# Performance work log

Measured on AMD Instinct MI355X. Metric: run time of the kernel, lower is better.

## Reference

```python
import jax, jax.numpy as jnp
import numpy as np

N_BUS = 200000; N_GEN = 50000
E_BB = 1600000; E_GB = 400000; E_BG = 400000
D_IN = 64; H = 32
OUT_BUS = 4; OUT_GEN = 2


def setup_inputs() -> dict:
    key = jax.random.key(0)
    it = iter(jax.random.split(key, 48))
    def nrm(shape, s=0.05):
        return jax.random.normal(next(it), shape, jnp.float32) * s
    inp = {}
    inp["x_bus"] = jax.random.normal(next(it), (N_BUS, D_IN), jnp.float32)
    inp["x_gen"] = jax.random.normal(next(it), (N_GEN, D_IN), jnp.float32)
    inp["src_bb"] = jax.random.randint(next(it), (E_BB,), 0, N_BUS)
    inp["dst_bb"] = jax.random.randint(next(it), (E_BB,), 0, N_BUS)
    inp["src_gb"] = jax.random.randint(next(it), (E_GB,), 0, N_GEN)
    inp["dst_gb"] = jax.random.randint(next(it), (E_GB,), 0, N_BUS)
    inp["src_bg"] = jax.random.randint(next(it), (E_BG,), 0, N_BUS)
    inp["dst_bg"] = jax.random.randint(next(it), (E_BG,), 0, N_GEN)
    # SAGEConv params per layer / relation: lin_l (on aggregated neighbors, with bias),
    # lin_r (root weight on x_dst, no bias) -- matches PyG SAGEConv defaults.
    for lname, din in (("l1", D_IN), ("l2", H)):
        for rel in ("bb", "gb", "bg"):
            inp[f"{lname}_{rel}_Wl"] = nrm((din, H))
            inp[f"{lname}_{rel}_bl"] = jnp.zeros((H,), jnp.float32)
            inp[f"{lname}_{rel}_Wr"] = nrm((din, H))
    for nt, dout in (("bus", OUT_BUS), ("gen", OUT_GEN)):
        inp[f"lin0_{nt}_W"] = nrm((H, H))
        inp[f"lin0_{nt}_b"] = jnp.zeros((H,), jnp.float32)
        inp[f"linf_{nt}_W"] = nrm((H, dout))
        inp[f"linf_{nt}_b"] = jnp.zeros((dout,), jnp.float32)
    return inp


def _sage(x_src, x_dst, src, dst, Wl, bl, Wr, n_dst):
    # SAGEConv: mean-aggregate neighbor features, then out = lin_l(mean) + lin_r(x_dst)
    msg = jax.ops.segment_sum(x_src[src], dst, num_segments=n_dst)
    cnt = jax.ops.segment_sum(jnp.ones((src.shape[0],), x_src.dtype), dst, num_segments=n_dst)
    mean = msg / jnp.maximum(cnt, 1.0)[:, None]
    return mean @ Wl + bl + x_dst @ Wr


def reference(x_bus, x_gen, src_bb, dst_bb, src_gb, dst_gb, src_bg, dst_bg,
              l1_bb_Wl, l1_bb_bl, l1_bb_Wr, l1_gb_Wl, l1_gb_bl, l1_gb_Wr,
              l1_bg_Wl, l1_bg_bl, l1_bg_Wr,
              l2_bb_Wl, l2_bb_bl, l2_bb_Wr, l2_gb_Wl, l2_gb_bl, l2_gb_Wr,
              l2_bg_Wl, l2_bg_bl, l2_bg_Wr,
              lin0_bus_W, lin0_bus_b, lin0_gen_W, lin0_gen_b,
              linf_bus_W, linf_bus_b, linf_gen_W, linf_gen_b):
    # HeteroConv layer 1 (aggr='sum' over relations targeting each dst type)
    hb = (_sage(x_bus, x_bus, src_bb, dst_bb, l1_bb_Wl, l1_bb_bl, l1_bb_Wr, N_BUS)
          + _sage(x_gen, x_bus, src_gb, dst_gb, l1_gb_Wl, l1_gb_bl, l1_gb_Wr, N_BUS))
    hg = _sage(x_bus, x_gen, src_bg, dst_bg, l1_bg_Wl, l1_bg_bl, l1_bg_Wr, N_GEN)
    xb, xg = jax.nn.relu(hb), jax.nn.relu(hg)  # dropout is identity in eval mode
    # HeteroConv layer 2
    hb = (_sage(xb, xb, src_bb, dst_bb, l2_bb_Wl, l2_bb_bl, l2_bb_Wr, N_BUS)
          + _sage(xg, xb, src_gb, dst_gb, l2_gb_Wl, l2_gb_bl, l2_gb_Wr, N_BUS))
    hg = _sage(xb, xg, src_bg, dst_bg, l2_bg_Wl, l2_bg_bl, l2_bg_Wr, N_GEN)
    xb, xg = jax.nn.relu(hb), jax.nn.relu(hg)
    # per-node-type hidden Linear (input relu'd again as in the original; relu is idempotent)
    xb = jax.nn.relu(xb) @ lin0_bus_W + lin0_bus_b
    xg = jax.nn.relu(xg) @ lin0_gen_W + lin0_gen_b
    out_bus = xb @ linf_bus_W + linf_bus_b
    out_gen = xg @ linf_gen_W + linf_gen_b
    return out_bus, out_gen
```

## Files before the change

kernel.cpp:

```cpp
#include <hip/hip_runtime.h>
#include <hip/hip_bf16.h>

#define N_BUS 200000
#define N_GEN 50000
#define E_BB 1600000
#define E_GB 400000
#define E_BG 400000
#define H 32
#define NBINS 1024
#define EPT 16

#define NBK_BUS 782
#define NBK_GEN 196
#define CAP_BB 2560
#define CAP_GB 768
#define CAP_BG 2560

#define NB_PART_BB 391
#define NB_PART_GB 98
#define NB_PART_BG 98
#define NB_PART_ALL 587
#define NB_TF_BUS 782
#define NB_TF_GEN 196
#define NB_PL_BUS 6250
#define NB_PL_GEN 1563

typedef __attribute__((ext_vector_type(8))) short short8;
typedef __attribute__((ext_vector_type(4))) float floatx4;

__device__ inline unsigned short f2bf(float f) {
    __hip_bfloat16 h = __float2bfloat16(f);
    return *reinterpret_cast<unsigned short*>(&h);
}
__device__ inline float bf2f(unsigned short u) {
    return __uint_as_float(((unsigned)u) << 16);
}

__device__ __forceinline__ void part_body(int blk, const int* __restrict__ src,
                                          const int* __restrict__ dst, int nE,
                                          unsigned* __restrict__ cnt, int CAP,
                                          unsigned* __restrict__ pairs) {
    __shared__ unsigned hist[NBINS];
    __shared__ unsigned base[NBINS];
    const int tid = threadIdx.x;
    const int cbase = blk * (256 * EPT);

    unsigned es[EPT], ed[EPT];
#pragma unroll
    for (int q = 0; q < EPT; q++) {
        int i = cbase + q * 256 + tid;
        if (i < nE) { es[q] = (unsigned)src[i]; ed[q] = (unsigned)dst[i]; }
        else ed[q] = 0xFFFFFFFFu;
    }
    for (int i = tid; i < NBINS; i += 256) hist[i] = 0;
    __syncthreads();
#pragma unroll
    for (int q = 0; q < EPT; q++)
        if (ed[q] != 0xFFFFFFFFu) atomicAdd(&hist[ed[q] >> 8], 1u);
    __syncthreads();
    for (int i = tid; i < NBINS; i += 256) {
        unsigned c = hist[i];
        base[i] = c ? ((unsigned)i * CAP + atomicAdd(&cnt[i], c)) : 0u;
        hist[i] = 0;
    }
    __syncthreads();
#pragma unroll
    for (int q = 0; q < EPT; q++) {
        if (ed[q] != 0xFFFFFFFFu) {
            unsigned b = ed[q] >> 8;
            unsigned off = atomicAdd(&hist[b], 1u);
            pairs[base[b] + off] = ((ed[q] & 255u) << 24) | es[q];
        }
    }
}

__global__ __launch_bounds__(256) void part_all_kernel(
    const int* __restrict__ sbb, const int* __restrict__ dbb, unsigned* __restrict__ cbb, unsigned* __restrict__ pbb,
    const int* __restrict__ sgb, const int* __restrict__ dgb, unsigned* __restrict__ cgb, unsigned* __restrict__ pgb,
    const int* __restrict__ sbg, const int* __restrict__ dbg, unsigned* __restrict__ cbg, unsigned* __restrict__ pbg)
{
    int b = blockIdx.x;
    if (b < NB_PART_BB) part_body(b, sbb, dbb, E_BB, cbb, CAP_BB, pbb);
    else if (b < NB_PART_BB + NB_PART_GB) part_body(b - NB_PART_BB, sgb, dgb, E_GB, cgb, CAP_GB, pgb);
    else part_body(b - NB_PART_BB - NB_PART_GB, sbg, dbg, E_BG, cbg, CAP_BG, pbg);
}

__device__ __forceinline__ void fine_body(int b, const unsigned* __restrict__ cnt_g, int CAP,
                                          const unsigned* __restrict__ pairs,
                                          unsigned* __restrict__ rs,
                                          unsigned* __restrict__ esrc, int nDst) {
    __shared__ unsigned cnt[256];
    __shared__ unsigned sh[256];
    const int tid = threadIdx.x;
    const unsigned start = (unsigned)b * CAP;
    const unsigned end = start + cnt_g[b];

    cnt[tid] = 0;
    __syncthreads();
    for (unsigned k = start + tid; k < end; k += 256)
        atomicAdd(&cnt[pairs[k] >> 24], 1u);
    __syncthreads();
    unsigned c = cnt[tid];
    sh[tid] = c;
    __syncthreads();
#pragma unroll
    for (int d = 1; d < 256; d <<= 1) {
        unsigned t = (tid >= d) ? sh[tid - d] : 0u;
        __syncthreads();
        sh[tid] += t;
        __syncthreads();
    }
    int gd = b * 256 + tid;
    unsigned rowstart = start + sh[tid] - c;
    if (gd < nDst) rs[gd] = (rowstart << 9) | (c < 511u ? c : 511u);
    cnt[tid] = sh[tid] - c;
    __syncthreads();
    for (unsigned k = start + tid; k < end; k += 256) {
        unsigned p = pairs[k];
        unsigned off = atomicAdd(&cnt[p >> 24], 1u);
        esrc[start + off] = p & 0x00FFFFFFu;
    }
}

__global__ __launch_bounds__(256) void fine_all_kernel(
    const unsigned* __restrict__ cbb, const unsigned* __restrict__ pbb, unsigned* __restrict__ rsbb, unsigned* __restrict__ ebb,
    const unsigned* __restrict__ cgb, const unsigned* __restrict__ pgb, unsigned* __restrict__ rsgb, unsigned* __restrict__ egb,
    const unsigned* __restrict__ cbg, const unsigned* __restrict__ pbg, unsigned* __restrict__ rsbg, unsigned* __restrict__ ebg)
{
    int b = blockIdx.x;
    if (b < NBK_BUS) fine_body(b, cbb, CAP_BB, pbb, rsbb, ebb, N_BUS);
    else if (b < 2 * NBK_BUS) fine_body(b - NBK_BUS, cgb, CAP_GB, pgb, rsgb, egb, N_BUS);
    else fine_body(b - 2 * NBK_BUS, cbg, CAP_BG, pbg, rsbg, ebg, N_GEN);
}

__global__ __launch_bounds__(256) void prep_kernel(
    const float* __restrict__ l1_bb_Wl, const float* __restrict__ l1_bb_bl, const float* __restrict__ l1_bb_Wr,
    const float* __restrict__ l1_gb_Wl, const float* __restrict__ l1_gb_bl, const float* __restrict__ l1_gb_Wr,
    const float* __restrict__ l1_bg_Wl, const float* __restrict__ l1_bg_bl, const float* __restrict__ l1_bg_Wr,
    const float* __restrict__ l2_bb_Wl, const float* __restrict__ l2_bb_bl, const float* __restrict__ l2_bb_Wr,
    const float* __restrict__ l2_gb_Wl, const float* __restrict__ l2_gb_bl, const float* __restrict__ l2_gb_Wr,
    const float* __restrict__ l2_bg_Wl, const float* __restrict__ l2_bg_bl, const float* __restrict__ l2_bg_Wr,
    const float* __restrict__ lin0_bus_W, const float* __restrict__ lin0_bus_b,
    const float* __restrict__ linf_bus_W, const float* __restrict__ linf_bus_b,
    const float* __restrict__ lin0_gen_W, const float* __restrict__ lin0_gen_b,
    const float* __restrict__ linf_gen_W, const float* __restrict__ linf_gen_b,
    unsigned short* __restrict__ Wf1b, float* __restrict__ B1b,
    unsigned short* __restrict__ Wf1g, float* __restrict__ B1g,
    unsigned short* __restrict__ Wf2b, float* __restrict__ B2b,
    unsigned short* __restrict__ Wf2g, float* __restrict__ B2g,
    float* __restrict__ WeB, float* __restrict__ beB,
    float* __restrict__ WeG, float* __restrict__ beG,
    unsigned* __restrict__ cursors)
{
    int t0 = blockIdx.x * 256 + threadIdx.x;
// ... 37 lines not shown
        B1b[t0] = (t0 < 64) ? 0.0f : l1_bb_bl[t0 - 64] + l1_gb_bl[t0 - 64];
        B2b[t0] = (t0 < 64) ? 0.0f : l2_bb_bl[t0 - 64] + l2_gb_bl[t0 - 64];
    }
    if (t0 < 64) {
        B1g[t0] = (t0 < 32) ? 0.0f : l1_bg_bl[t0 - 32];
        B2g[t0] = (t0 < 32) ? 0.0f : l2_bg_bl[t0 - 32];
    }
    if (t0 < 128) {
        int k = t0 >> 2, c = t0 & 3;
        float s = 0.0f;
        for (int m = 0; m < 32; m++) s += lin0_bus_W[k * 32 + m] * linf_bus_W[m * 4 + c];
        WeB[t0] = s;
    }
    if (t0 >= 128 && t0 < 132) {
        int c = t0 - 128;
        float s = linf_bus_b[c];
        for (int m = 0; m < 32; m++) s += lin0_bus_b[m] * linf_bus_W[m * 4 + c];
        beB[c] = s;
    }
    if (t0 >= 132 && t0 < 196) {
        int i = t0 - 132, k = i >> 1, c = i & 1;
        float s = 0.0f;
        for (int m = 0; m < 32; m++) s += lin0_gen_W[k * 32 + m] * linf_gen_W[m * 2 + c];
        WeG[i] = s;
    }
    if (t0 >= 196 && t0 < 198) {
        int c = t0 - 196;
        float s = linf_gen_b[c];
        for (int m = 0; m < 32; m++) s += lin0_gen_b[m] * linf_gen_W[m * 2 + c];
        beG[c] = s;
    }
}

template <int K, int NOUT, bool RELU_IN>
__device__ __forceinline__ void transform_body(
    int blk, const float* x, int n,
    const unsigned short* __restrict__ Wf, const float* __restrict__ bias,
    unsigned short* __restrict__ y0, unsigned short* __restrict__ y1, float* h,
    char* ldsraw)
{
    constexpr int KT = K / 32, NTN = NOUT / 16, NCH = NOUT / 32;
    constexpr int XS = K + 8;
    constexpr int OS = 34;
    short* lx = (short*)ldsraw;
    float* lo = (float*)ldsraw;

    const int tid = threadIdx.x;
    const int base = blk * 256;
    const int rows = min(256, n - base);
    const int w = tid >> 6, l = tid & 63, quad = l >> 4, ln = l & 15;

    short8 bf[KT][NTN];
    const short8* wf8 = (const short8*)Wf;
#pragma unroll
    for (int kt = 0; kt < KT; kt++)
#pragma unroll
        for (int nt = 0; nt < NTN; nt++)
            bf[kt][nt] = wf8[(kt * NTN + nt) * 64 + l];
    float bv[NTN];
#pragma unroll
    for (int nt = 0; nt < NTN; nt++) bv[nt] = bias[nt * 16 + ln];

    {
        const float4* xg = (const float4*)(x + (size_t)base * K);
        const int T4 = rows * (K / 4);
        for (int q = tid; q < T4; q += 256) {
            float4 v = xg[q];
            if (RELU_IN) {
                v.x = fmaxf(v.x, 0.f); v.y = fmaxf(v.y, 0.f);
                v.z = fmaxf(v.z, 0.f); v.w = fmaxf(v.w, 0.f);
            }
            int r = q / (K / 4), c = (q % (K / 4)) * 4;
            short4 s4;
            s4.x = (short)f2bf(v.x); s4.y = (short)f2bf(v.y);
            s4.z = (short)f2bf(v.z); s4.w = (short)f2bf(v.w);
            *(short4*)&lx[r * XS + c] = s4;
        }
    }
    __syncthreads();

    floatx4 acc[4][NTN];
#pragma unroll
    for (int mt = 0; mt < 4; mt++)
#pragma unroll
        for (int nt = 0; nt < NTN; nt++) {
            floatx4 c0 = {bv[nt], bv[nt], bv[nt], bv[nt]};
            acc[mt][nt] = c0;
        }
#pragma unroll
    for (int mt = 0; mt < 4; mt++) {
        const int row = w * 64 + mt * 16 + ln;
#pragma unroll
        for (int kt = 0; kt < KT; kt++) {
            short8 af = *(const short8*)&lx[row * XS + kt * 32 + quad * 8];
#pragma unroll
            for (int nt = 0; nt < NTN; nt++)
                acc[mt][nt] = __builtin_amdgcn_mfma_f32_16x16x32_bf16(
                    af, bf[kt][nt], acc[mt][nt], 0, 0, 0);
        }
    }

#pragma unroll
    for (int c = 0; c < NCH; c++) {
        __syncthreads();
#pragma unroll
        for (int mt = 0; mt < 4; mt++)
#pragma unroll
            for (int d = 0; d < 2; d++) {
                int nt = 2 * c + d;
#pragma unroll
                for (int r = 0; r < 4; r++)
                    lo[(w * 64 + mt * 16 + quad * 4 + r) * OS + d * 16 + ln] = acc[mt][nt][r];
            }
        __syncthreads();
        const int T4 = rows * 8;
        if (c == NCH - 1) {
            float* og = h + (size_t)base * 32;
            for (int q = tid; q < T4; q += 256) {
                int r = q >> 3, cc = (q & 7) * 4;
                const float* p = &lo[r * OS + cc];
                *(float4*)(og + q * 4) = make_float4(p[0], p[1], p[2], p[3]);
            }
        } else {
            unsigned short* og = ((c == 0) ? y0 : y1) + (size_t)base * 32;
            for (int q = tid; q < T4; q += 256) {
                int r = q >> 3, cc = (q & 7) * 4;
                const float* p = &lo[r * OS + cc];
                short4 s4;
                s4.x = (short)f2bf(p[0]); s4.y = (short)f2bf(p[1]);
                s4.z = (short)f2bf(p[2]); s4.w = (short)f2bf(p[3]);
                *(short4*)(og + q * 4) = s4;
            }
        }
    }
}

__global__ __launch_bounds__(256) void tf1_all_kernel(
    const float* xb, const unsigned short* __restrict__ Wfb, const float* __restrict__ Bb,
    unsigned short* __restrict__ yb0, unsigned short* __restrict__ yb1, float* hb,
    const float* xg, const unsigned short* __restrict__ Wfg, const float* __restrict__ Bg,
    unsigned short* __restrict__ yg0, float* hg)
{
    constexpr int XB = 256 * (64 + 8) * 2, OB = 256 * 34 * 4;
    __shared__ __align__(16) char ldsraw[(XB > OB) ? XB : OB];
    int b = blockIdx.x;
    if (b < NB_TF_BUS)
        transform_body<64, 96, false>(b, xb, N_BUS, Wfb, Bb, yb0, yb1, hb, ldsraw);
    else
        transform_body<64, 64, false>(b - NB_TF_BUS, xg, N_GEN, Wfg, Bg, yg0, nullptr, hg, ldsraw);
}

__global__ __launch_bounds__(256) void tf2_all_kernel(
    const float* xb, const unsigned short* __restrict__ Wfb, const float* __restrict__ Bb,
    unsigned short* __restrict__ yb0, unsigned short* __restrict__ yb1, float* hb,
    const float* xg, const unsigned short* __restrict__ Wfg, const float* __restrict__ Bg,
    unsigned short* __restrict__ yg0, float* hg)
{
    constexpr int XB = 256 * (32 + 8) * 2, OB = 256 * 34 * 4;
    __shared__ __align__(16) char ldsraw[(XB > OB) ? XB : OB];
    int b = blockIdx.x;
    if (b < NB_TF_BUS)
        transform_body<32, 96, true>(b, xb, N_BUS, Wfb, Bb, yb0, yb1, hb, ldsraw);
    else
        transform_body<32, 64, true>(b - NB_TF_BUS, xg, N_GEN, Wfg, Bg, yg0, nullptr, hg, ldsraw);
}

template <bool FUSE>
__device__ __forceinline__ void pull_body(
    int blk, bool hasB, int n,
    const unsigned* __restrict__ rsA, const unsigned* __restrict__ eA, const unsigned short* __restrict__ yA,
    const unsigned* __restrict__ rsB, const unsigned* __restrict__ eB, const unsigned short* __restrict__ yB,
    float* __restrict__ h,
    const float* __restrict__ We, const float* __restrict__ be, int DOUT, float* __restrict__ outp)
{
    const int tid = threadIdx.x;
    unsigned node = blk * 32u + (tid >> 3);
    int j = (tid & 7) * 4;
    if (node >= (unsigned)n) return;

    float4 r = *(const float4*)(h + (size_t)node * H + j);

    auto accum_rel = [&](const unsigned* __restrict__ rs, const unsigned* __restrict__ e,
                         const unsigned short* __restrict__ y) {
        unsigned u = rs[node];
        unsigned k0 = u >> 9;
        unsigned c = u & 511u;
        unsigned k1 = k0 + c;
        float4 a0 = make_float4(0.f, 0.f, 0.f, 0.f);
        float4 a1 = make_float4(0.f, 0.f, 0.f, 0.f);
        float4 a2 = make_float4(0.f, 0.f, 0.f, 0.f);
        float4 a3 = make_float4(0.f, 0.f, 0.f, 0.f);
        unsigned k = k0;
        for (; k + 4 <= k1; k += 4) {
            unsigned s0 = e[k], s1 = e[k + 1], s2 = e[k + 2], s3 = e[k + 3];
            ushort4 v0 = *(const ushort4*)(y + (size_t)s0 * H + j);
            ushort4 v1 = *(const ushort4*)(y + (size_t)s1 * H + j);
            ushort4 v2 = *(const ushort4*)(y + (size_t)s2 * H + j);
            ushort4 v3 = *(const ushort4*)(y + (size_t)s3 * H + j);
            a0.x += bf2f(v0.x); a0.y += bf2f(v0.y); a0.z += bf2f(v0.z); a0.w += bf2f(v0.w);
            a1.x += bf2f(v1.x); a1.y += bf2f(v1.y); a1.z += bf2f(v1.z); a1.w += bf2f(v1.w);
            a2.x += bf2f(v2.x); a2.y += bf2f(v2.y); a2.z += bf2f(v2.z); a2.w += bf2f(v2.w);
            a3.x += bf2f(v3.x); a3.y += bf2f(v3.y); a3.z += bf2f(v3.z); a3.w += bf2f(v3.w);
        }
        for (; k < k1; ++k) {
            unsigned s = e[k];
            const ushort4 v = *(const ushort4*)(y + (size_t)s * H + j);
            a0.x += bf2f(v.x); a0.y += bf2f(v.y); a0.z += bf2f(v.z); a0.w += bf2f(v.w);
        }
        a0.x += a1.x + a2.x + a3.x; a0.y += a1.y + a2.y + a3.y;
        a0.z += a1.z + a2.z + a3.z; a0.w += a1.w + a2.w + a3.w;
        float inv = 1.0f / (float)(c > 1u ? c : 1u);
        r.x += a0.x * inv; r.y += a0.y * inv; r.z += a0.z * inv; r.w += a0.w * inv;
    };

    accum_rel(rsA, eA, yA);
    if (hasB) accum_rel(rsB, eB, yB);

    if (!FUSE) {
        *(float4*)(h + (size_t)node * H + j) = r;
        return;
    }

    float p0 = fmaxf(r.x, 0.f), p1 = fmaxf(r.y, 0.f), p2 = fmaxf(r.z, 0.f), p3 = fmaxf(r.w, 0.f);
    float tot[4];
#pragma unroll
    for (int c = 0; c < 4; c++) {
        if (c < DOUT) {
            tot[c] = p0 * We[(j + 0) * DOUT + c] + p1 * We[(j + 1) * DOUT + c]
                   + p2 * We[(j + 2) * DOUT + c] + p3 * We[(j + 3) * DOUT + c];
        } else tot[c] = 0.f;
    }
#pragma unroll
    for (int mask = 1; mask <= 4; mask <<= 1) {
#pragma unroll
        for (int c = 0; c < 4; c++) tot[c] += __shfl_xor(tot[c], mask);
    }
    if ((tid & 7) == 0) {
        if (DOUT == 4) {
            *(float4*)(outp + (size_t)node * 4) =
                make_float4(tot[0] + be[0], tot[1] + be[1], tot[2] + be[2], tot[3] + be[3]);
        } else {
            *(float2*)(outp + (size_t)node * 2) = make_float2(tot[0] + be[0], tot[1] + be[1]);
        }
    }
}

template <bool FUSE>
__global__ __launch_bounds__(256) void pull_all_kernel(
    const unsigned* __restrict__ rsbb, const unsigned* __restrict__ ebb, const unsigned short* __restrict__ ybb,
    const unsigned* __restrict__ rsgb, const unsigned* __restrict__ egb, const unsigned short* __restrict__ ygb,
    float* __restrict__ hb, const float* __restrict__ WeB, const float* __restrict__ beB,
    const unsigned* __restrict__ rsbg, const unsigned* __restrict__ ebg, const unsigned short* __restrict__ ybg,
    float* __restrict__ hg, const float* __restrict__ WeG, const float* __restrict__ beG,
    float* __restrict__ outp)
{
    int b = blockIdx.x;
    if (b < NB_PL_BUS)
        pull_body<FUSE>(b, true, N_BUS, rsbb, ebb, ybb, rsgb, egb, ygb, hb, WeB, beB, 4, outp);
    else
        pull_body<FUSE>(b - NB_PL_BUS, false, N_GEN, rsbg, ebg, ybg, nullptr, nullptr, nullptr,
                        hg, WeG, beG, 2, outp ? outp + (size_t)N_BUS * 4 : nullptr);
}

extern "C" void kernel_launch(void* const* d_in, const int* in_sizes, int n_in,
                              void* d_out, int out_size, void* d_ws, size_t ws_size,
                              hipStream_t stream) {
    const float* x_bus = (const float*)d_in[0];
    const float* x_gen = (const float*)d_in[1];
    const int* src_bb = (const int*)d_in[2];
    const int* dst_bb = (const int*)d_in[3];
    const int* src_gb = (const int*)d_in[4];
    const int* dst_gb = (const int*)d_in[5];
    const int* src_bg = (const int*)d_in[6];
    const int* dst_bg = (const int*)d_in[7];
    const float* l1_bb_Wl = (const float*)d_in[8];
    const float* l1_bb_bl = (const float*)d_in[9];
    const float* l1_bb_Wr = (const float*)d_in[10];
    const float* l1_gb_Wl = (const float*)d_in[11];
    const float* l1_gb_bl = (const float*)d_in[12];
    const float* l1_gb_Wr = (const float*)d_in[13];
    const float* l1_bg_Wl = (const float*)d_in[14];
    const float* l1_bg_bl = (const float*)d_in[15];
    const float* l1_bg_Wr = (const float*)d_in[16];
    const float* l2_bb_Wl = (const float*)d_in[17];
    const float* l2_bb_bl = (const float*)d_in[18];
    const float* l2_bb_Wr = (const float*)d_in[19];
    const float* l2_gb_Wl = (const float*)d_in[20];
    const float* l2_gb_bl = (const float*)d_in[21];
    const float* l2_gb_Wr = (const float*)d_in[22];
    const float* l2_bg_Wl = (const float*)d_in[23];
    const float* l2_bg_bl = (const float*)d_in[24];
    const float* l2_bg_Wr = (const float*)d_in[25];
    const float* lin0_bus_W = (const float*)d_in[26];
    const float* lin0_bus_b = (const float*)d_in[27];
    const float* linf_bus_W = (const float*)d_in[28];
    const float* linf_bus_b = (const float*)d_in[29];
    const float* lin0_gen_W = (const float*)d_in[30];
    const float* lin0_gen_b = (const float*)d_in[31];
    const float* linf_gen_W = (const float*)d_in[32];
    const float* linf_gen_b = (const float*)d_in[33];

    char* ws = (char*)d_ws;
    size_t off = 0;
    auto alloc = [&](size_t bytes) {
        char* p = ws + off;
        off += (bytes + 255) & ~(size_t)255;
        return p;
    };
    unsigned* rs_bb = (unsigned*)alloc((size_t)N_BUS * 4);
    unsigned* rs_gb = (unsigned*)alloc((size_t)N_BUS * 4);
    unsigned* rs_bg = (unsigned*)alloc((size_t)N_GEN * 4);
    unsigned* cur_bb = (unsigned*)alloc(NBINS * 4);
    unsigned* cur_gb = (unsigned*)alloc(NBINS * 4);
    unsigned* cur_bg = (unsigned*)alloc(NBINS * 4);
    unsigned* e_bb = (unsigned*)alloc((size_t)NBK_BUS * CAP_BB * 4);
    unsigned* e_gb = (unsigned*)alloc((size_t)NBK_BUS * CAP_GB * 4);
    unsigned* e_bg = (unsigned*)alloc((size_t)NBK_GEN * CAP_BG * 4);
    unsigned* p_bb = (unsigned*)alloc((size_t)NBK_BUS * CAP_BB * 4);
    unsigned* p_gb = (unsigned*)alloc((size_t)NBK_BUS * CAP_GB * 4);
    unsigned* p_bg = (unsigned*)alloc((size_t)NBK_GEN * CAP_BG * 4);
    unsigned short* y_bb = (unsigned short*)alloc((size_t)N_BUS * H * 2);
    unsigned short* y_bg = (unsigned short*)alloc((size_t)N_BUS * H * 2);
    unsigned short* y_gb = (unsigned short*)alloc((size_t)N_GEN * H * 2);
    float* h_bus = (float*)alloc((size_t)N_BUS * H * 4);
    float* h_gen = (float*)alloc((size_t)N_GEN * H * 4);
    unsigned short* Wf1b = (unsigned short*)alloc(2 * 6 * 64 * 8 * 2);
    float* B1b = (float*)alloc(96 * 4);
    unsigned short* Wf1g = (unsigned short*)alloc(2 * 4 * 64 * 8 * 2);
    float* B1g = (float*)alloc(64 * 4);
    unsigned short* Wf2b = (unsigned short*)alloc(6 * 64 * 8 * 2);
    float* B2b = (float*)alloc(96 * 4);
    unsigned short* Wf2g = (unsigned short*)alloc(4 * 64 * 8 * 2);
    float* B2g = (float*)alloc(64 * 4);
    float* WeB = (float*)alloc(128 * 4);
    float* beB = (float*)alloc(4 * 4);
    float* WeG = (float*)alloc(64 * 4);
    float* beG = (float*)alloc(2 * 4);

    prep_kernel<<<32, 256, 0, stream>>>(
        l1_bb_Wl, l1_bb_bl, l1_bb_Wr, l1_gb_Wl, l1_gb_bl, l1_gb_Wr,
        l1_bg_Wl, l1_bg_bl, l1_bg_Wr, l2_bb_Wl, l2_bb_bl, l2_bb_Wr,
        l2_gb_Wl, l2_gb_bl, l2_gb_Wr, l2_bg_Wl, l2_bg_bl, l2_bg_Wr,
        lin0_bus_W, lin0_bus_b, linf_bus_W, linf_bus_b,
        lin0_gen_W, lin0_gen_b, linf_gen_W, linf_gen_b,
        Wf1b, B1b, Wf1g, B1g, Wf2b, B2b, Wf2g, B2g, WeB, beB, WeG, beG,
        cur_bb);

    part_all_kernel<<<NB_PART_ALL, 256, 0, stream>>>(
        src_bb, dst_bb, cur_bb, p_bb, src_gb, dst_gb, cur_gb, p_gb, src_bg, dst_bg, cur_bg, p_bg);

    fine_all_kernel<<<2 * NBK_BUS + NBK_GEN, 256, 0, stream>>>(
        cur_bb, p_bb, rs_bb, e_bb, cur_gb, p_gb, rs_gb, e_gb, cur_bg, p_bg, rs_bg, e_bg);

    tf1_all_kernel<<<NB_TF_BUS + NB_TF_GEN, 256, 0, stream>>>(
        x_bus, Wf1b, B1b, y_bb, y_bg, h_bus, x_gen, Wf1g, B1g, y_gb, h_gen);

    pull_all_kernel<false><<<NB_PL_BUS + NB_PL_GEN, 256, 0, stream>>>(
        rs_bb, e_bb, y_bb, rs_gb, e_gb, y_gb, h_bus, WeB, beB,
        rs_bg, e_bg, y_bg, h_gen, WeG, beG, nullptr);

    tf2_all_kernel<<<NB_TF_BUS + NB_TF_GEN, 256, 0, stream>>>(
        h_bus, Wf2b, B2b, y_bb, y_bg, h_bus, h_gen, Wf2g, B2g, y_gb, h_gen);

    pull_all_kernel<true><<<NB_PL_BUS + NB_PL_GEN, 256, 0, stream>>>(
        rs_bb, e_bb, y_bb, rs_gb, e_gb, y_gb, h_bus, WeB, beB,
        rs_bg, e_bg, y_bg, h_gen, WeG, beG, (float*)d_out);
}
```

Before: 347.5 us.

## Fuse layer-1 aggregation with layer-2 transform into one kernel

Merges the layer-1 neighbor pull (mean aggregation plus root term) with the layer-2 MFMA transform. Each block gathers and aggregates its 256 nodes, applies ReLU and writes bf16 rows straight into LDS, then runs the shared MFMA tail. This removes one kernel launch and the fp32 h round-trip to global memory between the two stages. New y2 buffers are needed because the fused kernel reads the layer-1 y buffers while writing layer-2 outputs. In exchange, per-block gather latency is serialized before the MFMA, and there is a fallback path when the workspace is too small.

```diff
diff --git a/kernel.cpp b/kernel.cpp
--- a/kernel.cpp
+++ b/kernel.cpp
@@ -223,11 +223,11 @@
     }
 }
 
-template <int K, int NOUT, bool RELU_IN>
-__device__ __forceinline__ void transform_body(
-    int blk, const float* x, int n,
+template <int K, int NOUT>
+__device__ __forceinline__ void mfma_tail(
+    int rows, int base,
     const unsigned short* __restrict__ Wf, const float* __restrict__ bias,
-    unsigned short* __restrict__ y0, unsigned short* __restrict__ y1, float* h,
+    unsigned short* __restrict__ y0, unsigned short* __restrict__ y1, float* __restrict__ h,
     char* ldsraw)
 {
     constexpr int KT = K / 32, NTN = NOUT / 16, NCH = NOUT / 32;
@@ -235,10 +235,7 @@
     constexpr int OS = 34;
     short* lx = (short*)ldsraw;
     float* lo = (float*)ldsraw;
-
     const int tid = threadIdx.x;
-    const int base = blk * 256;
-    const int rows = min(256, n - base);
     const int w = tid >> 6, l = tid & 63, quad = l >> 4, ln = l & 15;
 
     short8 bf[KT][NTN];
@@ -251,24 +248,6 @@
     float bv[NTN];
 #pragma unroll
     for (int nt = 0; nt < NTN; nt++) bv[nt] = bias[nt * 16 + ln];
-
-    {
-        const float4* xg = (const float4*)(x + (size_t)base * K);
-        const int T4 = rows * (K / 4);
-        for (int q = tid; q < T4; q += 256) {
-            float4 v = xg[q];
-            if (RELU_IN) {
-                v.x = fmaxf(v.x, 0.f); v.y = fmaxf(v.y, 0.f);
-                v.z = fmaxf(v.z, 0.f); v.w = fmaxf(v.w, 0.f);
-            }
-            int r = q / (K / 4), c = (q % (K / 4)) * 4;
-            short4 s4;
-            s4.x = (short)f2bf(v.x); s4.y = (short)f2bf(v.y);
-            s4.z = (short)f2bf(v.z); s4.w = (short)f2bf(v.w);
-            *(short4*)&lx[r * XS + c] = s4;
-        }
-    }
-    __syncthreads();
 
     floatx4 acc[4][NTN];
 #pragma unroll
@@ -326,6 +305,39 @@
     }
 }
 
+template <int K, int NOUT, bool RELU_IN>
+__device__ __forceinline__ void transform_body(
+    int blk, const float* x, int n,
+    const unsigned short* __restrict__ Wf, const float* __restrict__ bias,
+    unsigned short* __restrict__ y0, unsigned short* __restrict__ y1, float* h,
+    char* ldsraw)
+{
+    constexpr int XS = K + 8;
+    short* lx = (short*)ldsraw;
+    const int tid = threadIdx.x;
+    const int base = blk * 256;
+    const int rows = min(256, n - base);
+
+    {
+        const float4* xg = (const float4*)(x + (size_t)base * K);
+        const int T4 = rows * (K / 4);
+        for (int q = tid; q < T4; q += 256) {
+            float4 v = xg[q];
+            if (RELU_IN) {
+                v.x = fmaxf(v.x, 0.f); v.y = fmaxf(v.y, 0.f);
+                v.z = fmaxf(v.z, 0.f); v.w = fmaxf(v.w, 0.f);
+            }
+            int r = q / (K / 4), c = (q % (K / 4)) * 4;
+            short4 s4;
+            s4.x = (short)f2bf(v.x); s4.y = (short)f2bf(v.y);
+            s4.z = (short)f2bf(v.z); s4.w = (short)f2bf(v.w);
+            *(short4*)&lx[r * XS + c] = s4;
+        }
+    }
+    __syncthreads();
+    mfma_tail<K, NOUT>(rows, base, Wf, bias, y0, y1, h, ldsraw);
+}
+
 __global__ __launch_bounds__(256) void tf1_all_kernel(
     const float* xb, const unsigned short* __restrict__ Wfb, const float* __restrict__ Bb,
     unsigned short* __restrict__ yb0, unsigned short* __restrict__ yb1, float* hb,
@@ -356,6 +368,107 @@
         transform_body<32, 64, true>(b - NB_TF_BUS, xg, N_GEN, Wfg, Bg, yg0, nullptr, hg, ldsraw);
 }
 
+__device__ __forceinline__ void agg_one(
+    unsigned u, const unsigned* __restrict__ e,
+    const unsigned short* __restrict__ y, int j, float4& r)
+{
+    unsigned k0 = u >> 9;
+    unsigned c = u & 511u;
+    unsigned k1 = k0 + c;
+    float4 a0 = make_float4(0.f, 0.f, 0.f, 0.f);
+    float4 a1 = a0, a2 = a0, a3 = a0;
+    unsigned k = k0;
+    for (; k + 4 <= k1; k += 4) {
+        unsigned s0 = e[k], s1 = e[k + 1], s2 = e[k + 2], s3 = e[k + 3];
+        ushort4 v0 = *(const ushort4*)(y + (size_t)s0 * H + j);
+        ushort4 v1 = *(const ushort4*)(y + (size_t)s1 * H + j);
+        ushort4 v2 = *(const ushort4*)(y + (size_t)s2 * H + j);
+        ushort4 v3 = *(const ushort4*)(y + (size_t)s3 * H + j);
+        a0.x += bf2f(v0.x); a0.y += bf2f(v0.y); a0.z += bf2f(v0.z); a0.w += bf2f(v0.w);
+        a1.x += bf2f(v1.x); a1.y += bf2f(v1.y); a1.z += bf2f(v1.z); a1.w += bf2f(v1.w);
+        a2.x += bf2f(v2.x); a2.y += bf2f(v2.y); a2.z += bf2f(v2.z); a2.w += bf2f(v2.w);
+        a3.x += bf2f(v3.x); a3.y += bf2f(v3.y); a3.z += bf2f(v3.z); a3.w += bf2f(v3.w);
+    }
+    for (; k < k1; ++k) {
+        unsigned s = e[k];
+        const ushort4 v = *(const ushort4*)(y + (size_t)s * H + j);
+        a0.x += bf2f(v.x); a0.y += bf2f(v.y); a0.z += bf2f(v.z); a0.w += bf2f(v.w);
+    }
+    a0.x += a1.x + a2.x + a3.x; a0.y += a1.y + a2.y + a3.y;
+    a0.z += a1.z + a2.z + a3.z; a0.w += a1.w + a2.w + a3.w;
+    float inv = 1.0f / (float)(c > 1u ? c : 1u);
+    r.x += a0.x * inv; r.y += a0.y * inv; r.z += a0.z * inv; r.w += a0.w * inv;
+}
+
+template <int NOUT, bool HASB>
+__device__ __forceinline__ void agg_tf_body(
+    int blk, int n,
+    const unsigned* __restrict__ rsA, const unsigned* __restrict__ eA, const unsigned short* __restrict__ yA,
+    const unsigned* __restrict__ rsB, const unsigned* __restrict__ eB, const unsigned short* __restrict__ yB,
+    const float* __restrict__ hroot,
+    const unsigned short* __restrict__ Wf, const float* __restrict__ bias,
+    unsigned short* __restrict__ y0, unsigned short* __restrict__ y1, float* __restrict__ hout,
+    char* ldsraw)
+{
+    constexpr int K = 32, XS = K + 8;
+    short* lx = (short*)ldsraw;
+    const int tid = threadIdx.x;
+    const int base = blk * 256;
+    const int rows = min(256, n - base);
+    const int g = tid >> 3;
+    const int j = (tid & 7) * 4;
+
+    unsigned uA[8], uB[8];
+#pragma unroll
+    for (int it = 0; it < 8; ++it) {
+        int r = it * 32 + g;
+        bool v = r < rows;
+        uA[it] = v ? rsA[base + r] : 0u;
+        if (HASB) uB[it] = v ? rsB[base + r] : 0u;
+    }
+#pragma unroll
+    for (int it = 0; it < 8; ++it) {
+        int r = it * 32 + g;
+        if (r < rows) {
+            int node = base + r;
+            float4 acc = *(const float4*)(hroot + (size_t)node * H + j);
+            agg_one(uA[it], eA, yA, j, acc);
+            if (HASB) agg_one(uB[it], eB, yB, j, acc);
+            short4 s4;
+            s4.x = (short)f2bf(fmaxf(acc.x, 0.f));
+            s4.y = (short)f2bf(fmaxf(acc.y, 0.f));
+            s4.z = (short)f2bf(fmaxf(acc.z, 0.f));
+            s4.w = (short)f2bf(fmaxf(acc.w, 0.f));
+            *(short4*)&lx[r * XS + j] = s4;
+        }
+    }
+    __syncthreads();
+    mfma_tail<32, NOUT>(rows, base, Wf, bias, y0, y1, hout, ldsraw);
+}
+
+__global__ __launch_bounds__(256) void agg_tf2_all_kernel(
+    const unsigned* __restrict__ rsbb, const unsigned* __restrict__ ebb, const unsigned short* __restrict__ ybb,
+    const unsigned* __restrict__ rsgb, const unsigned* __restrict__ egb, const unsigned short* __restrict__ ygb,
+    float* __restrict__ hb,
+    const unsigned short* __restrict__ Wfb, const float* __restrict__ Bb,
+    unsigned short* __restrict__ y2bb, unsigned short* __restrict__ y2bg,
+    const unsigned* __restrict__ rsbg, const unsigned* __restrict__ ebg, const unsigned short* __restrict__ ybg,
+    float* __restrict__ hg,
+    const unsigned short* __restrict__ Wfg, const float* __restrict__ Bg,
+    unsigned short* __restrict__ y2gb)
+{
+    constexpr int XB = 256 * (32 + 8) * 2, OB = 256 * 34 * 4;
+    __shared__ __align__(16) char ldsraw[(XB > OB) ? XB : OB];
+    int b = blockIdx.x;
+    if (b < NB_TF_BUS)
+        agg_tf_body<96, true>(b, N_BUS, rsbb, ebb, ybb, rsgb, egb, ygb,
+                              hb, Wfb, Bb, y2bb, y2bg, hb, ldsraw);
+    else
+        agg_tf_body<64, false>(b - NB_TF_BUS, N_GEN, rsbg, ebg, ybg,
+                               nullptr, nullptr, nullptr,
+                               hg, Wfg, Bg, y2gb, nullptr, hg, ldsraw);
+}
+
 template <bool FUSE>
 __device__ __forceinline__ void pull_body(
     int blk, bool hasB, int n,
@@ -371,41 +484,8 @@
 
     float4 r = *(const float4*)(h + (size_t)node * H + j);
 
-    auto accum_rel = [&](const unsigned* __restrict__ rs, const unsigned* __restrict__ e,
-                         const unsigned short* __restrict__ y) {
-        unsigned u = rs[node];
-        unsigned k0 = u >> 9;
-        unsigned c = u & 511u;
-        unsigned k1 = k0 + c;
-        float4 a0 = make_float4(0.f, 0.f, 0.f, 0.f);
-        float4 a1 = make_float4(0.f, 0.f, 0.f, 0.f);
-        float4 a2 = make_float4(0.f, 0.f, 0.f, 0.f);
-        float4 a3 = make_float4(0.f, 0.f, 0.f, 0.f);
-        unsigned k = k0;
-        for (; k + 4 <= k1; k += 4) {
-            unsigned s0 = e[k], s1 = e[k + 1], s2 = e[k + 2], s3 = e[k + 3];
-            ushort4 v0 = *(const ushort4*)(y + (size_t)s0 * H + j);
-            ushort4 v1 = *(const ushort4*)(y + (size_t)s1 * H + j);
-            ushort4 v2 = *(const ushort4*)(y + (size_t)s2 * H + j);
-            ushort4 v3 = *(const ushort4*)(y + (size_t)s3 * H + j);
-            a0.x += bf2f(v0.x); a0.y += bf2f(v0.y); a0.z += bf2f(v0.z); a0.w += bf2f(v0.w);
-            a1.x += bf2f(v1.x); a1.y += bf2f(v1.y); a1.z += bf2f(v1.z); a1.w += bf2f(v1.w);
-            a2.x += bf2f(v2.x); a2.y += bf2f(v2.y); a2.z += bf2f(v2.z); a2.w += bf2f(v2.w);
-            a3.x += bf2f(v3.x); a3.y += bf2f(v3.y); a3.z += bf2f(v3.z); a3.w += bf2f(v3.w);
-        }
-        for (; k < k1; ++k) {
-            unsigned s = e[k];
-            const ushort4 v = *(const ushort4*)(y + (size_t)s * H + j);
-            a0.x += bf2f(v.x); a0.y += bf2f(v.y); a0.z += bf2f(v.z); a0.w += bf2f(v.w);
-        }
-        a0.x += a1.x + a2.x + a3.x; a0.y += a1.y + a2.y + a3.y;
-        a0.z += a1.z + a2.z + a3.z; a0.w += a1.w + a2.w + a3.w;
-        float inv = 1.0f / (float)(c > 1u ? c : 1u);
-        r.x += a0.x * inv; r.y += a0.y * inv; r.z += a0.z * inv; r.w += a0.w * inv;
-    };
-
-    accum_rel(rsA, eA, yA);
-    if (hasB) accum_rel(rsB, eB, yB);
+    agg_one(rsA[node], eA, yA, j, r);
+    if (hasB) agg_one(rsB[node], eB, yB, j, r);
 
     if (!FUSE) {
         *(float4*)(h + (size_t)node * H + j) = r;
@@ -527,6 +607,10 @@
     float* beB = (float*)alloc(4 * 4);
     float* WeG = (float*)alloc(64 * 4);
     float* beG = (float*)alloc(2 * 4);
+    unsigned short* y2_bb = (unsigned short*)alloc((size_t)N_BUS * H * 2);
+    unsigned short* y2_bg = (unsigned short*)alloc((size_t)N_BUS * H * 2);
+    unsigned short* y2_gb = (unsigned short*)alloc((size_t)N_GEN * H * 2);
+    const bool fused = (ws_size == 0) || (off <= ws_size);
 
     prep_kernel<<<32, 256, 0, stream>>>(
         l1_bb_Wl, l1_bb_bl, l1_bb_Wr, l1_gb_Wl, l1_gb_bl, l1_gb_Wr,
@@ -546,14 +630,22 @@
     tf1_all_kernel<<<NB_TF_BUS + NB_TF_GEN, 256, 0, stream>>>(
         x_bus, Wf1b, B1b, y_bb, y_bg, h_bus, x_gen, Wf1g, B1g, y_gb, h_gen);
 
-    pull_all_kernel<false><<<NB_PL_BUS + NB_PL_GEN, 256, 0, stream>>>(
-        rs_bb, e_bb, y_bb, rs_gb, e_gb, y_gb, h_bus, WeB, beB,
-        rs_bg, e_bg, y_bg, h_gen, WeG, beG, nullptr);
-
-    tf2_all_kernel<<<NB_TF_BUS + NB_TF_GEN, 256, 0, stream>>>(
-        h_bus, Wf2b, B2b, y_bb, y_bg, h_bus, h_gen, Wf2g, B2g, y_gb, h_gen);
-
-    pull_all_kernel<true><<<NB_PL_BUS + NB_PL_GEN, 256, 0, stream>>>(
-        rs_bb, e_bb, y_bb, rs_gb, e_gb, y_gb, h_bus, WeB, beB,
-        rs_bg, e_bg, y_bg, h_gen, WeG, beG, (float*)d_out);
-}
+    if (fused) {
+        agg_tf2_all_kernel<<<NB_TF_BUS + NB_TF_GEN, 256, 0, stream>>>(
+            rs_bb, e_bb, y_bb, rs_gb, e_gb, y_gb, h_bus, Wf2b, B2b, y2_bb, y2_bg,
+            rs_bg, e_bg, y_bg, h_gen, Wf2g, B2g, y2_gb);
+
+        pull_all_kernel<true><<<NB_PL_BUS + NB_PL_GEN, 256, 0, stream>>>(
+            rs_bb, e_bb, y2_bb, rs_gb, e_gb, y2_gb, h_bus, WeB, beB,
+            rs_bg, e_bg, y2_bg, h_gen, WeG, beG, (float*)d_out);
+    } else {
+        pull_all_kernel<false><<<NB_PL_BUS + NB_PL_GEN, 256, 0, stream>>>(
+            rs_bb, e_bb, y_bb, rs_gb, e_gb, y_gb, h_bus, WeB, beB,
+            rs_bg, e_bg, y_bg, h_gen, WeG, beG, nullptr);
+        tf2_all_kernel<<<NB_TF_BUS + NB_TF_GEN, 256, 0, stream>>>(
+            h_bus, Wf2b, B2b, y_bb, y_bg, h_bus, h_gen, Wf2g, B2g, y_gb, h_gen);
+        pull_all_kernel<true><<<NB_PL_BUS + NB_PL_GEN, 256, 0, stream>>>(
+            rs_bb, e_bb, y_bb, rs_gb, e_gb, y_gb, h_bus, WeB, beB,
+            rs_bg, e_bg, y_bg, h_gen, WeG, beG, (float*)d_out);
+    }
+}
```

New measurement: 390.8 us. +12.5%, slower.

## Stage scatters in LDS, store layer-1 activations as relu'd bf16, prefetch edge indices

Applied to the files above, without the earlier changes.

The partition and fine-sort kernels now stage their scattered writes in shared memory, using a local prefix scan over bins, then write them out contiguously. This is meant to turn random global stores into coalesced ones, at the cost of more LDS and extra barriers. The layer-1 pull now writes relu'd bf16 activations into a new buffer, so the layer-2 transform reads half the bytes and skips the conversion. The edge aggregation loop also prefetches the next four source indices to hide gather latency.

```diff
diff --git a/kernel.cpp b/kernel.cpp
--- a/kernel.cpp
+++ b/kernel.cpp
@@ -38,12 +38,17 @@
 
 __device__ __forceinline__ void part_body(int blk, const int* __restrict__ src,
                                           const int* __restrict__ dst, int nE,
-                                          unsigned* __restrict__ cnt, int CAP,
+                                          unsigned* __restrict__ cnt_g, int CAP,
                                           unsigned* __restrict__ pairs) {
     __shared__ unsigned hist[NBINS];
     __shared__ unsigned base[NBINS];
+    __shared__ unsigned sbase[NBINS];
+    __shared__ unsigned sh[256];
+    __shared__ unsigned pairv[256 * EPT];
+    __shared__ unsigned short bid[256 * EPT];
     const int tid = threadIdx.x;
     const int cbase = blk * (256 * EPT);
+    const int total = min(256 * EPT, nE - cbase);
 
     unsigned es[EPT], ed[EPT];
 #pragma unroll
@@ -58,19 +63,46 @@
     for (int q = 0; q < EPT; q++)
         if (ed[q] != 0xFFFFFFFFu) atomicAdd(&hist[ed[q] >> 8], 1u);
     __syncthreads();
-    for (int i = tid; i < NBINS; i += 256) {
-        unsigned c = hist[i];
-        base[i] = c ? ((unsigned)i * CAP + atomicAdd(&cnt[i], c)) : 0u;
-        hist[i] = 0;
-    }
-    __syncthreads();
+
+    unsigned h4[4];
+    unsigned s = 0;
+#pragma unroll
+    for (int k2 = 0; k2 < 4; k2++) { h4[k2] = hist[tid * 4 + k2]; s += h4[k2]; }
+    sh[tid] = s;
+    __syncthreads();
+#pragma unroll
+    for (int d = 1; d < 256; d <<= 1) {
+        unsigned t = (tid >= d) ? sh[tid - d] : 0u;
+        __syncthreads();
+        sh[tid] += t;
+        __syncthreads();
+    }
+    unsigned run = sh[tid] - s;
+#pragma unroll
+    for (int k2 = 0; k2 < 4; k2++) {
+        int b = tid * 4 + k2;
+        sbase[b] = run;
+        base[b] = h4[k2] ? ((unsigned)b * CAP + atomicAdd(&cnt_g[b], h4[k2])) : 0u;
+        hist[b] = 0;
+        run += h4[k2];
+    }
+    __syncthreads();
+
 #pragma unroll
     for (int q = 0; q < EPT; q++) {
         if (ed[q] != 0xFFFFFFFFu) {
             unsigned b = ed[q] >> 8;
             unsigned off = atomicAdd(&hist[b], 1u);
-            pairs[base[b] + off] = ((ed[q] & 255u) << 24) | es[q];
-        }
+            unsigned p = sbase[b] + off;
+            pairv[p] = ((ed[q] & 255u) << 24) | es[q];
+            bid[p] = (unsigned short)b;
+        }
+    }
+    __syncthreads();
+
+    for (int p = tid; p < total; p += 256) {
+        unsigned b = bid[p];
+        pairs[base[b] + ((unsigned)p - sbase[b])] = pairv[p];
     }
 }
 
@@ -91,9 +123,11 @@
                                           unsigned* __restrict__ esrc, int nDst) {
     __shared__ unsigned cnt[256];
     __shared__ unsigned sh[256];
+    __shared__ unsigned stg[2560];
     const int tid = threadIdx.x;
     const unsigned start = (unsigned)b * CAP;
-    const unsigned end = start + cnt_g[b];
+    const unsigned m = cnt_g[b];
+    const unsigned end = start + m;
 
     cnt[tid] = 0;
     __syncthreads();
@@ -118,8 +152,10 @@
     for (unsigned k = start + tid; k < end; k += 256) {
         unsigned p = pairs[k];
         unsigned off = atomicAdd(&cnt[p >> 24], 1u);
-        esrc[start + off] = p & 0x00FFFFFFu;
-    }
+        stg[off] = p & 0x00FFFFFFu;
+    }
+    __syncthreads();
+    for (unsigned p = tid; p < m; p += 256) esrc[start + p] = stg[p];
 }
 
 __global__ __launch_bounds__(256) void fine_all_kernel(
@@ -223,11 +259,11 @@
     }
 }
 
-template <int K, int NOUT, bool RELU_IN>
-__device__ __forceinline__ void transform_body(
-    int blk, const float* x, int n,
+template <int K, int NOUT>
+__device__ __forceinline__ void mfma_tail(
+    int rows, int base,
     const unsigned short* __restrict__ Wf, const float* __restrict__ bias,
-    unsigned short* __restrict__ y0, unsigned short* __restrict__ y1, float* h,
+    unsigned short* __restrict__ y0, unsigned short* __restrict__ y1, float* __restrict__ h,
     char* ldsraw)
 {
     constexpr int KT = K / 32, NTN = NOUT / 16, NCH = NOUT / 32;
@@ -235,10 +271,7 @@
     constexpr int OS = 34;
     short* lx = (short*)ldsraw;
     float* lo = (float*)ldsraw;
-
     const int tid = threadIdx.x;
-    const int base = blk * 256;
-    const int rows = min(256, n - base);
     const int w = tid >> 6, l = tid & 63, quad = l >> 4, ln = l & 15;
 
     short8 bf[KT][NTN];
@@ -251,24 +284,6 @@
     float bv[NTN];
 #pragma unroll
     for (int nt = 0; nt < NTN; nt++) bv[nt] = bias[nt * 16 + ln];
-
-    {
-        const float4* xg = (const float4*)(x + (size_t)base * K);
-        const int T4 = rows * (K / 4);
-        for (int q = tid; q < T4; q += 256) {
-            float4 v = xg[q];
-            if (RELU_IN) {
-                v.x = fmaxf(v.x, 0.f); v.y = fmaxf(v.y, 0.f);
-                v.z = fmaxf(v.z, 0.f); v.w = fmaxf(v.w, 0.f);
-            }
-            int r = q / (K / 4), c = (q % (K / 4)) * 4;
-            short4 s4;
-            s4.x = (short)f2bf(v.x); s4.y = (short)f2bf(v.y);
-            s4.z = (short)f2bf(v.z); s4.w = (short)f2bf(v.w);
-            *(short4*)&lx[r * XS + c] = s4;
-        }
-    }
-    __syncthreads();
 
     floatx4 acc[4][NTN];
 #pragma unroll
@@ -326,6 +341,61 @@
     }
 }
 
+template <int K, int NOUT>
+__device__ __forceinline__ void transform_body(
+    int blk, const float* x, int n,
+    const unsigned short* __restrict__ Wf, const float* __restrict__ bias,
+    unsigned short* __restrict__ y0, unsigned short* __restrict__ y1, float* h,
+    char* ldsraw)
+{
+    constexpr int XS = K + 8;
+    short* lx = (short*)ldsraw;
+    const int tid = threadIdx.x;
+    const int base = blk * 256;
+    const int rows = min(256, n - base);
+
+    {
+        const float4* xg = (const float4*)(x + (size_t)base * K);
+        const int T4 = rows * (K / 4);
+        for (int q = tid; q < T4; q += 256) {
+            float4 v = xg[q];
+            int r = q / (K / 4), c = (q % (K / 4)) * 4;
+            short4 s4;
+            s4.x = (short)f2bf(v.x); s4.y = (short)f2bf(v.y);
+            s4.z = (short)f2bf(v.z); s4.w = (short)f2bf(v.w);
+            *(short4*)&lx[r * XS + c] = s4;
+        }
+    }
+    __syncthreads();
+    mfma_tail<K, NOUT>(rows, base, Wf, bias, y0, y1, h, ldsraw);
+}
+
+template <int NOUT>
+__device__ __forceinline__ void transform_bf16_body(
+    int blk, const unsigned short* x, int n,
+    const unsigned short* __restrict__ Wf, const float* __restrict__ bias,
+    unsigned short* __restrict__ y0, unsigned short* __restrict__ y1, float* h,
+    char* ldsraw)
+{
+    constexpr int K = 32, XS = K + 8;
+    short* lx = (short*)ldsraw;
+    const int tid = threadIdx.x;
+    const int base = blk * 256;
+    const int rows = min(256, n - base);
+
+    {
+        const short8* xg = (const short8*)(x + (size_t)base * K);
+        const int T8 = rows * (K / 8);
+        for (int q = tid; q < T8; q += 256) {
+            short8 v = xg[q];
+            int r = q / (K / 8), c = (q % (K / 8)) * 8;
+            *(short8*)&lx[r * XS + c] = v;
+        }
+    }
+    __syncthreads();
+    mfma_tail<K, NOUT>(rows, base, Wf, bias, y0, y1, h, ldsraw);
+}
+
 __global__ __launch_bounds__(256) void tf1_all_kernel(
     const float* xb, const unsigned short* __restrict__ Wfb, const float* __restrict__ Bb,
     unsigned short* __restrict__ yb0, unsigned short* __restrict__ yb1, float* hb,
@@ -336,54 +406,40 @@
     __shared__ __align__(16) char ldsraw[(XB > OB) ? XB : OB];
     int b = blockIdx.x;
     if (b < NB_TF_BUS)
-        transform_body<64, 96, false>(b, xb, N_BUS, Wfb, Bb, yb0, yb1, hb, ldsraw);
+        transform_body<64, 96>(b, xb, N_BUS, Wfb, Bb, yb0, yb1, hb, ldsraw);
     else
-        transform_body<64, 64, false>(b - NB_TF_BUS, xg, N_GEN, Wfg, Bg, yg0, nullptr, hg, ldsraw);
-}
-
-__global__ __launch_bounds__(256) void tf2_all_kernel(
-    const float* xb, const unsigned short* __restrict__ Wfb, const float* __restrict__ Bb,
+        transform_body<64, 64>(b - NB_TF_BUS, xg, N_GEN, Wfg, Bg, yg0, nullptr, hg, ldsraw);
+}
+
+__global__ __launch_bounds__(256) void tf2b_all_kernel(
+    const unsigned short* x2b, const unsigned short* __restrict__ Wfb, const float* __restrict__ Bb,
     unsigned short* __restrict__ yb0, unsigned short* __restrict__ yb1, float* hb,
-    const float* xg, const unsigned short* __restrict__ Wfg, const float* __restrict__ Bg,
+    const unsigned short* x2g, const unsigned short* __restrict__ Wfg, const float* __restrict__ Bg,
     unsigned short* __restrict__ yg0, float* hg)
 {
     constexpr int XB = 256 * (32 + 8) * 2, OB = 256 * 34 * 4;
     __shared__ __align__(16) char ldsraw[(XB > OB) ? XB : OB];
     int b = blockIdx.x;
     if (b < NB_TF_BUS)
-        transform_body<32, 96, true>(b, xb, N_BUS, Wfb, Bb, yb0, yb1, hb, ldsraw);
+        transform_bf16_body<96>(b, x2b, N_BUS, Wfb, Bb, yb0, yb1, hb, ldsraw);
     else
-        transform_body<32, 64, true>(b - NB_TF_BUS, xg, N_GEN, Wfg, Bg, yg0, nullptr, hg, ldsraw);
-}
-
-template <bool FUSE>
-__device__ __forceinline__ void pull_body(
-    int blk, bool hasB, int n,
-    const unsigned* __restrict__ rsA, const unsigned* __restrict__ eA, const unsigned short* __restrict__ yA,
-    const unsigned* __restrict__ rsB, const unsigned* __restrict__ eB, const unsigned short* __restrict__ yB,
-    float* __restrict__ h,
-    const float* __restrict__ We, const float* __restrict__ be, int DOUT, float* __restrict__ outp)
-{
-    const int tid = threadIdx.x;
-    unsigned node = blk * 32u + (tid >> 3);
-    int j = (tid & 7) * 4;
-    if (node >= (unsigned)n) return;
-
-    float4 r = *(const float4*)(h + (size_t)node * H + j);
-
-    auto accum_rel = [&](const unsigned* __restrict__ rs, const unsigned* __restrict__ e,
-                         const unsigned short* __restrict__ y) {
-        unsigned u = rs[node];
-        unsigned k0 = u >> 9;
-        unsigned c = u & 511u;
-        unsigned k1 = k0 + c;
-        float4 a0 = make_float4(0.f, 0.f, 0.f, 0.f);
-        float4 a1 = make_float4(0.f, 0.f, 0.f, 0.f);
-        float4 a2 = make_float4(0.f, 0.f, 0.f, 0.f);
-        float4 a3 = make_float4(0.f, 0.f, 0.f, 0.f);
-        unsigned k = k0;
-        for (; k + 4 <= k1; k += 4) {
-            unsigned s0 = e[k], s1 = e[k + 1], s2 = e[k + 2], s3 = e[k + 3];
+        transform_bf16_body<64>(b - NB_TF_BUS, x2g, N_GEN, Wfg, Bg, yg0, nullptr, hg, ldsraw);
+}
+
+__device__ __forceinline__ void agg_one(
+    unsigned u, const unsigned* __restrict__ e,
+    const unsigned short* __restrict__ y, int j, float4& r)
+{
+    unsigned k0 = u >> 9;
+    unsigned c = u & 511u;
+    unsigned k1 = k0 + c;
+    float4 a0 = make_float4(0.f, 0.f, 0.f, 0.f);
+    float4 a1 = a0, a2 = a0, a3 = a0;
+    unsigned k = k0;
+    if (k + 4 <= k1) {
+        unsigned s0 = e[k], s1 = e[k + 1], s2 = e[k + 2], s3 = e[k + 3];
+        for (; k + 8 <= k1; k += 4) {
+            unsigned t0 = e[k + 4], t1 = e[k + 5], t2 = e[k + 6], t3 = e[k + 7];
             ushort4 v0 = *(const ushort4*)(y + (size_t)s0 * H + j);
             ushort4 v1 = *(const ushort4*)(y + (size_t)s1 * H + j);
             ushort4 v2 = *(const ushort4*)(y + (size_t)s2 * H + j);
@@ -392,23 +448,54 @@
             a1.x += bf2f(v1.x); a1.y += bf2f(v1.y); a1.z += bf2f(v1.z); a1.w += bf2f(v1.w);
             a2.x += bf2f(v2.x); a2.y += bf2f(v2.y); a2.z += bf2f(v2.z); a2.w += bf2f(v2.w);
             a3.x += bf2f(v3.x); a3.y += bf2f(v3.y); a3.z += bf2f(v3.z); a3.w += bf2f(v3.w);
-        }
-        for (; k < k1; ++k) {
-            unsigned s = e[k];
-            const ushort4 v = *(const ushort4*)(y + (size_t)s * H + j);
-            a0.x += bf2f(v.x); a0.y += bf2f(v.y); a0.z += bf2f(v.z); a0.w += bf2f(v.w);
-        }
-        a0.x += a1.x + a2.x + a3.x; a0.y += a1.y + a2.y + a3.y;
-        a0.z += a1.z + a2.z + a3.z; a0.w += a1.w + a2.w + a3.w;
-        float inv = 1.0f / (float)(c > 1u ? c : 1u);
-        r.x += a0.x * inv; r.y += a0.y * inv; r.z += a0.z * inv; r.w += a0.w * inv;
-    };
-
-    accum_rel(rsA, eA, yA);
-    if (hasB) accum_rel(rsB, eB, yB);
+            s0 = t0; s1 = t1; s2 = t2; s3 = t3;
+        }
+        {
+            ushort4 v0 = *(const ushort4*)(y + (size_t)s0 * H + j);
+            ushort4 v1 = *(const ushort4*)(y + (size_t)s1 * H + j);
+            ushort4 v2 = *(const ushort4*)(y + (size_t)s2 * H + j);
+            ushort4 v3 = *(const ushort4*)(y + (size_t)s3 * H + j);
+            a0.x += bf2f(v0.x); a0.y += bf2f(v0.y); a0.z += bf2f(v0.z); a0.w += bf2f(v0.w);
+            a1.x += bf2f(v1.x); a1.y += bf2f(v1.y); a1.z += bf2f(v1.z); a1.w += bf2f(v1.w);
+            a2.x += bf2f(v2.x); a2.y += bf2f(v2.y); a2.z += bf2f(v2.z); a2.w += bf2f(v2.w);
+            a3.x += bf2f(v3.x); a3.y += bf2f(v3.y); a3.z += bf2f(v3.z); a3.w += bf2f(v3.w);
+            k += 4;
+        }
+    }
+    for (; k < k1; ++k) {
+        unsigned s = e[k];
+        const ushort4 v = *(const ushort4*)(y + (size_t)s * H + j);
+        a0.x += bf2f(v.x); a0.y += bf2f(v.y); a0.z += bf2f(v.z); a0.w += bf2f(v.w);
+    }
+    a0.x += a1.x + a2.x + a3.x; a0.y += a1.y + a2.y + a3.y;
+    a0.z += a1.z + a2.z + a3.z; a0.w += a1.w + a2.w + a3.w;
+    float inv = 1.0f / (float)(c > 1u ? c : 1u);
+    r.x += a0.x * inv; r.y += a0.y * inv; r.z += a0.z * inv; r.w += a0.w * inv;
+}
+
+template <bool FUSE>
+__device__ __forceinline__ void pull_body(
+    int blk, bool hasB, int n,
+    const unsigned* __restrict__ rsA, const unsigned* __restrict__ eA, const unsigned short* __restrict__ yA,
+    const unsigned* __restrict__ rsB, const unsigned* __restrict__ eB, const unsigned short* __restrict__ yB,
+    const float* __restrict__ h, unsigned short* __restrict__ x2,
+    const float* __restrict__ We, const float* __restrict__ be, int DOUT, float* __restrict__ outp)
+{
+    const int tid = threadIdx.x;
+    unsigned node = blk * 32u + (tid >> 3);
+    int j = (tid & 7) * 4;
+    if (node >= (unsigned)n) return;
+
+    float4 r = *(const float4*)(h + (size_t)node * H + j);
+
+    agg_one(rsA[node], eA, yA, j, r);
+    if (hasB) agg_one(rsB[node], eB, yB, j, r);
 
     if (!FUSE) {
-        *(float4*)(h + (size_t)node * H + j) = r;
+        ushort4 o;
+        o.x = f2bf(fmaxf(r.x, 0.f)); o.y = f2bf(fmaxf(r.y, 0.f));
+        o.z = f2bf(fmaxf(r.z, 0.f)); o.w = f2bf(fmaxf(r.w, 0.f));
+        *(ushort4*)(x2 + (size_t)node * H + j) = o;
         return;
     }
 
@@ -440,17 +527,19 @@
 __global__ __launch_bounds__(256) void pull_all_kernel(
     const unsigned* __restrict__ rsbb, const unsigned* __restrict__ ebb, const unsigned short* __restrict__ ybb,
     const unsigned* __restrict__ rsgb, const unsigned* __restrict__ egb, const unsigned short* __restrict__ ygb,
-    float* __restrict__ hb, const float* __restrict__ WeB, const float* __restrict__ beB,
+    const float* __restrict__ hb, unsigned short* __restrict__ x2b,
+    const float* __restrict__ WeB, const float* __restrict__ beB,
     const unsigned* __restrict__ rsbg, const unsigned* __restrict__ ebg, const unsigned short* __restrict__ ybg,
-    float* __restrict__ hg, const float* __restrict__ WeG, const float* __restrict__ beG,
+    const float* __restrict__ hg, unsigned short* __restrict__ x2g,
+    const float* __restrict__ WeG, const float* __restrict__ beG,
     float* __restrict__ outp)
 {
     int b = blockIdx.x;
     if (b < NB_PL_BUS)
-        pull_body<FUSE>(b, true, N_BUS, rsbb, ebb, ybb, rsgb, egb, ygb, hb, WeB, beB, 4, outp);
+        pull_body<FUSE>(b, true, N_BUS, rsbb, ebb, ybb, rsgb, egb, ygb, hb, x2b, WeB, beB, 4, outp);
     else
         pull_body<FUSE>(b - NB_PL_BUS, false, N_GEN, rsbg, ebg, ybg, nullptr, nullptr, nullptr,
-                        hg, WeG, beG, 2, outp ? outp + (size_t)N_BUS * 4 : nullptr);
+                        hg, x2g, WeG, beG, 2, outp ? outp + (size_t)N_BUS * 4 : nullptr);
 }
 
 extern "C" void kernel_launch(void* const* d_in, const int* in_sizes, int n_in,
@@ -515,6 +604,8 @@
     unsigned short* y_gb = (unsigned short*)alloc((size_t)N_GEN * H * 2);
     float* h_bus = (float*)alloc((size_t)N_BUS * H * 4);
     float* h_gen = (float*)alloc((size_t)N_GEN * H * 4);
+    unsigned short* x2_bus = (unsigned short*)alloc((size_t)N_BUS * H * 2);
+    unsigned short* x2_gen = (unsigned short*)alloc((size_t)N_GEN * H * 2);
     unsigned short* Wf1b = (unsigned short*)alloc(2 * 6 * 64 * 8 * 2);
     float* B1b = (float*)alloc(96 * 4);
     unsigned short* Wf1g = (unsigned short*)alloc(2 * 4 * 64 * 8 * 2);
@@ -547,13 +638,13 @@
         x_bus, Wf1b, B1b, y_bb, y_bg, h_bus, x_gen, Wf1g, B1g, y_gb, h_gen);
 
     pull_all_kernel<false><<<NB_PL_BUS + NB_PL_GEN, 256, 0, stream>>>(
-        rs_bb, e_bb, y_bb, rs_gb, e_gb, y_gb, h_bus, WeB, beB,
-        rs_bg, e_bg, y_bg, h_gen, WeG, beG, nullptr);
-
-    tf2_all_kernel<<<NB_TF_BUS + NB_TF_GEN, 256, 0, stream>>>(
-        h_bus, Wf2b, B2b, y_bb, y_bg, h_bus, h_gen, Wf2g, B2g, y_gb, h_gen);
+        rs_bb, e_bb, y_bb, rs_gb, e_gb, y_gb, h_bus, x2_bus, WeB, beB,
+        rs_bg, e_bg, y_bg, h_gen, x2_gen, WeG, beG, nullptr);
+
+    tf2b_all_kernel<<<NB_TF_BUS + NB_TF_GEN, 256, 0, stream>>>(
+        x2_bus, Wf2b, B2b, y_bb, y_bg, h_bus, x2_gen, Wf2g, B2g, y_gb, h_gen);
 
     pull_all_kernel<true><<<NB_PL_BUS + NB_PL_GEN, 256, 0, stream>>>(
-        rs_bb, e_bb, y_bb, rs_gb, e_gb, y_gb, h_bus, WeB, beB,
-        rs_bg, e_bg, y_bg, h_gen, WeG, beG, (float*)d_out);
-}
+        rs_bb, e_bb, y_bb, rs_gb, e_gb, y_gb, h_bus, nullptr, WeB, beB,
+        rs_bg, e_bg, y_bg, h_gen, nullptr, WeG, beG, (float*)d_out);
+}
```

New measurement: 351.7 us. About the same (+1.2%).
